# Kernel optimization log

Hardware: AMD Instinct MI355X
Metric: run time of the kernel (lower is better)

The kernel has to match this reference:

```python
import jax, jax.numpy as jnp
import numpy as np

B, N, D, D_OUT = 8, 2048, 1024, 1024

def setup_inputs() -> dict:
    key = jax.random.key(0)
    k1, k2, k3, k4, k5 = jax.random.split(key, 5)
    x = jax.random.normal(k1, (B, N, D), dtype=jnp.float32)
    # nn.Linear params: weight [out, in], bias [out]
    W_attn = jax.random.normal(k2, (D, D), dtype=jnp.float32) / np.sqrt(D)
    b_attn = jax.random.normal(k3, (D,), dtype=jnp.float32) * 0.01
    W_out = jax.random.normal(k4, (D_OUT, D), dtype=jnp.float32) / np.sqrt(D)
    b_out = jax.random.normal(k5, (D_OUT,), dtype=jnp.float32) * 0.01
    return {"x": x, "W_attn": W_attn, "b_attn": b_attn, "W_out": W_out, "b_out": b_out}

def reference(x, W_attn, b_attn, W_out, b_out):
    # query = x; key = attention_linear(x); value = output_linear(x)
    key = jnp.einsum('bnd,kd->bnk', x, W_attn) + b_attn   # [B,N,D]
    value = jnp.einsum('bnd,od->bno', x, W_out) + b_out   # [B,N,D_OUT]
    scale = 1.0 / np.sqrt(x.shape[-1]).astype(np.float32)
    scores = jnp.einsum('bqd,bkd->bqk', x, key) * scale   # [B,N,N]
    attn = jax.nn.softmax(scores, axis=-1)
    return jnp.einsum('bqk,bko->bqo', attn, value)        # [B,N,D_OUT]
```

## Files before the change

kernel.cpp:

```cpp
#include <hip/hip_runtime.h>
#include <hip/hip_bf16.h>
#include <cstdio>

typedef __bf16 bf16_t;
typedef __bf16 bf16x8 __attribute__((ext_vector_type(8)));
typedef __bf16 bf16x4 __attribute__((ext_vector_type(4)));
typedef float  f32x16 __attribute__((ext_vector_type(16)));

#define TM 128
#define TN 128
#define BK 32

__global__ __launch_bounds__(256)
void cvt_f32_bf16(const float* __restrict__ in, bf16_t* __restrict__ out, int n)
{
    for (int i = (blockIdx.x * 256 + threadIdx.x) * 4; i < n; i += gridDim.x * 256 * 4) {
        const float4 v = *(const float4*)(in + i);
        bf16x4 o;
        o[0] = (bf16_t)v.x; o[1] = (bf16_t)v.y; o[2] = (bf16_t)v.z; o[3] = (bf16_t)v.w;
        *(bf16x4*)(out + i) = o;
    }
}


__device__ __forceinline__ void stage_tiles(
    const bf16_t* __restrict__ Ab, const bf16_t* __restrict__ Bb,
    bf16_t* As, bf16_t* Bs, int k0, int K, int t, int w)
{
    const int src_c = (t & 3) ^ ((t >> 3) & 3);
#pragma unroll
    for (int rd = 0; rd < 2; rd++) {
        const int row = rd * 64 + (t >> 2);
        const bf16_t* ga = Ab + (size_t)row * K + k0 + src_c * 8;
        __builtin_amdgcn_global_load_lds(
            (const __attribute__((address_space(1))) void*)ga,
            (__attribute__((address_space(3))) void*)(&As[(rd * 64 + w * 16) * 32]),
            16, 0, 0);
        const bf16_t* gb = Bb + (size_t)row * K + k0 + src_c * 8;
        __builtin_amdgcn_global_load_lds(
            (const __attribute__((address_space(1))) void*)gb,
            (__attribute__((address_space(3))) void*)(&Bs[(rd * 64 + w * 16) * 32]),
            16, 0, 0);
    }
}

__device__ __forceinline__ int frag_idx(int row, int c)
{
    return row * 32 + ((c ^ ((row >> 1) & 3)) * 8);
}

template <int MODE>
__global__ __launch_bounds__(256)
void gemm_nt(const bf16_t* __restrict__ A, const bf16_t* __restrict__ Bm,
             void* __restrict__ Cv, float scale, int Ncols, int K,
             long long strideA, long long strideB, long long strideC,
             int tiles_m, int tiles_n)
{
    __shared__ bf16_t As[TM * BK];
    __shared__ bf16_t Bs[TN * BK];

    const int t    = threadIdx.x;
    const int w    = t >> 6;
    const int lane = t & 63;
    const int wm = w >> 1, wn = w & 1;
    const int lm = lane & 31;
    const int lk = lane >> 5;

    const int per_batch = tiles_m * tiles_n;
    const int batch = blockIdx.x / per_batch;
    const int rest  = blockIdx.x % per_batch;
    const int tm    = rest % tiles_m;
    const int tn    = rest / tiles_m;

    const bf16_t* Ab = A + (size_t)batch * strideA + (size_t)tm * TM * K;
    const bf16_t* Bb = Bm + (size_t)batch * strideB + (size_t)tn * TN * K;

    f32x16 acc[2][2];
#pragma unroll
    for (int i = 0; i < 2; i++)
#pragma unroll
        for (int j = 0; j < 2; j++)
#pragma unroll
            for (int e = 0; e < 16; e++) acc[i][j][e] = 0.f;

    for (int k0 = 0; k0 < K; k0 += BK) {
        stage_tiles(Ab, Bb, As, Bs, k0, K, t, w);
        __syncthreads();

        bf16x8 af[2][2], bf[2][2];
#pragma unroll
        for (int ks = 0; ks < 2; ks++) {
#pragma unroll
            for (int mt = 0; mt < 2; mt++)
                af[ks][mt] = *(const bf16x8*)&As[frag_idx(wm * 64 + mt * 32 + lm, ks * 2 + lk)];
#pragma unroll
            for (int nt = 0; nt < 2; nt++)
                bf[ks][nt] = *(const bf16x8*)&Bs[frag_idx(wn * 64 + nt * 32 + lm, ks * 2 + lk)];
        }
#pragma unroll
        for (int ks = 0; ks < 2; ks++)
#pragma unroll
            for (int mt = 0; mt < 2; mt++)
#pragma unroll
                for (int nt = 0; nt < 2; nt++)
                    acc[mt][nt] = __builtin_amdgcn_mfma_f32_32x32x16_bf16(
                        af[ks][mt], bf[ks][nt], acc[mt][nt], 0, 0, 0);
        __syncthreads();
    }

#pragma unroll
    for (int mt = 0; mt < 2; mt++)
#pragma unroll
        for (int nt = 0; nt < 2; nt++) {
            const int colg = tn * TN + wn * 64 + nt * 32 + lm;
#pragma unroll
            for (int rg = 0; rg < 4; rg++) {
                const int rowg = tm * TM + wm * 64 + mt * 32 + rg * 8 + 4 * lk;
                if (MODE == 2) {
                    bf16_t* p = (bf16_t*)Cv + (size_t)batch * strideC
                                  + (size_t)rowg * Ncols + colg;
#pragma unroll
                    for (int j = 0; j < 4; j++)
                        p[(size_t)j * Ncols] = (bf16_t)(acc[mt][nt][rg * 4 + j] * scale);
                } else {
                    float* p = (float*)Cv + (size_t)batch * strideC
                                  + (size_t)rowg * Ncols + colg;
#pragma unroll
                    for (int j = 0; j < 4; j++)
                        p[(size_t)j * Ncols] = acc[mt][nt][rg * 4 + j];
                }
            }
        }
}

__global__ __launch_bounds__(256)
void gemm_kv(const bf16_t* __restrict__ A,
             const bf16_t* __restrict__ Wa, const bf16_t* __restrict__ Wo,
             const float* __restrict__ ba, const float* __restrict__ bo,
             bf16_t* __restrict__ key, bf16_t* __restrict__ vT,
             int Nn, int Dd, int K)
{
    __shared__ bf16_t As[TM * BK];
    __shared__ bf16_t Bs[TN * BK];

    const int t    = threadIdx.x;
    const int w    = t >> 6;
    const int lane = t & 63;
    const int wm = w >> 1, wn = w & 1;
    const int lm = lane & 31;
    const int lk = lane >> 5;

    const int tiles_m = Nn / TM;
    const int per_batch = tiles_m * 16;
    const int batch = blockIdx.x / per_batch;
    const int rest  = blockIdx.x % per_batch;
    const int tm    = rest % tiles_m;
    const int tn    = rest / tiles_m;
    const bool isK  = (tn < 8);

    const bf16_t* Ab = A + (size_t)batch * Nn * K + (size_t)tm * TM * K;
    const bf16_t* Bb = (isK ? Wa + (size_t)tn * TN * K
                            : Wo + (size_t)(tn - 8) * TN * K);
    const float* bias = isK ? ba : bo;

    f32x16 acc[2][2];
#pragma unroll
    for (int i = 0; i < 2; i++)
#pragma unroll
        for (int j = 0; j < 2; j++)
#pragma unroll
            for (int e = 0; e < 16; e++) acc[i][j][e] = 0.f;

    for (int k0 = 0; k0 < K; k0 += BK) {
        stage_tiles(Ab, Bb, As, Bs, k0, K, t, w);
        __syncthreads();

        bf16x8 af[2][2], bf[2][2];
#pragma unroll
        for (int ks = 0; ks < 2; ks++) {
#pragma unroll
            for (int mt = 0; mt < 2; mt++)
                af[ks][mt] = *(const bf16x8*)&As[frag_idx(wm * 64 + mt * 32 + lm, ks * 2 + lk)];
#pragma unroll
            for (int nt = 0; nt < 2; nt++)
                bf[ks][nt] = *(const bf16x8*)&Bs[frag_idx(wn * 64 + nt * 32 + lm, ks * 2 + lk)];
        }
#pragma unroll
        for (int ks = 0; ks < 2; ks++)
#pragma unroll
            for (int mt = 0; mt < 2; mt++)
#pragma unroll
                for (int nt = 0; nt < 2; nt++)
                    acc[mt][nt] = __builtin_amdgcn_mfma_f32_32x32x16_bf16(
                        af[ks][mt], bf[ks][nt], acc[mt][nt], 0, 0, 0);
        __syncthreads();
    }

#pragma unroll
    for (int mt = 0; mt < 2; mt++)
#pragma unroll
        for (int nt = 0; nt < 2; nt++) {
            const int cw = (tn & 7) * TN + wn * 64 + nt * 32 + lm;
            const float bv = bias[cw];
#pragma unroll
            for (int rg = 0; rg < 4; rg++) {
                const int rowg = tm * TM + wm * 64 + mt * 32 + rg * 8 + 4 * lk;
                if (isK) {
                    bf16_t* p = key + (size_t)batch * Nn * Dd + (size_t)rowg * Dd + cw;
#pragma unroll
                    for (int j = 0; j < 4; j++)
                        p[(size_t)j * Dd] = (bf16_t)(acc[mt][nt][rg * 4 + j] + bv);
                } else {
                    bf16_t* p = vT + (size_t)batch * Dd * Nn + (size_t)cw * Nn + rowg;
                    bf16x4 pk;
#pragma unroll
                    for (int j = 0; j < 4; j++)
                        pk[j] = (bf16_t)(acc[mt][nt][rg * 4 + j] + bv);
                    *(bf16x4*)p = pk;
                }
            }
        }
}

__global__ __launch_bounds__(256)
void softmax_rows(bf16_t* __restrict__ S)
{
    __shared__ float red[8];
    const int t = threadIdx.x;
    const int w = t >> 6;
    const int lane = t & 63;
    bf16_t* p = S + (size_t)blockIdx.x * 2048;

    bf16x8 v = *(const bf16x8*)&p[t * 8];
    float x[8];
    float m = -1e30f;
#pragma unroll
    for (int i = 0; i < 8; i++) { x[i] = (float)v[i]; m = fmaxf(m, x[i]); }
#pragma unroll
    for (int off = 32; off >= 1; off >>= 1) m = fmaxf(m, __shfl_xor(m, off));
    if (lane == 0) red[w] = m;
    __syncthreads();
    m = fmaxf(fmaxf(red[0], red[1]), fmaxf(red[2], red[3]));

    float s = 0.f;
#pragma unroll
    for (int i = 0; i < 8; i++) { x[i] = __expf(x[i] - m); s += x[i]; }
#pragma unroll
    for (int off = 32; off >= 1; off >>= 1) s += __shfl_xor(s, off);
    if (lane == 0) red[4 + w] = s;
    __syncthreads();
    const float inv = 1.f / (red[4] + red[5] + red[6] + red[7]);

    bf16x8 o;
#pragma unroll
    for (int i = 0; i < 8; i++) o[i] = (bf16_t)(x[i] * inv);
    *(bf16x8*)&p[t * 8] = o;
}

extern "C" void kernel_launch(void* const* d_in, const int* in_sizes, int n_in,
                              void* d_out, int out_size, void* d_ws, size_t ws_size,
                              hipStream_t stream)
{
    const int Bn = 8, Nn = 2048, Dd = 1024;

    const float* x  = (const float*)d_in[0];
    const float* Wa = (const float*)d_in[1];
    const float* ba = (const float*)d_in[2];
    const float* Wo = (const float*)d_in[3];
    const float* bo = (const float*)d_in[4];
    float* out = (float*)d_out;

    const size_t nX = (size_t)Bn * Nn * Dd;
    const size_t nW = (size_t)Dd * Dd;
    const size_t nS = (size_t)Bn * Nn * Nn;

    bf16_t* xb  = (bf16_t*)d_ws;
    bf16_t* Wab = xb + nX;
    bf16_t* Wob = Wab + nW;
    bf16_t* key = Wob + nW;
    bf16_t* vT  = key + nX;
    bf16_t* S   = vT + nX;
    const size_t needed = (nX * 3 + nW * 2 + nS) * sizeof(bf16_t);
    if (ws_size < needed)
        fprintf(stderr, "kernel_launch: ws too small: have %zu need %zu\n", ws_size, needed);

    const dim3 blk(256);
    const long long sXN = (long long)Nn * Dd;
    const long long sS  = (long long)Nn * Nn;
    const long long sVT = (long long)Dd * Nn;

    cvt_f32_bf16<<<dim3(16384), blk, 0, stream>>>(x, xb, (int)nX);
    cvt_f32_bf16<<<dim3(1024), blk, 0, stream>>>(Wa, Wab, (int)nW);
    cvt_f32_bf16<<<dim3(1024), blk, 0, stream>>>(Wo, Wob, (int)nW);

    gemm_kv<<<dim3(Bn * 16 * 16), blk, 0, stream>>>(
        xb, Wab, Wob, ba, bo, key, vT, Nn, Dd, Dd);

    gemm_nt<2><<<dim3(Bn * 16 * 16), blk, 0, stream>>>(
        xb, key, S, 0.03125f, Nn, Dd, sXN, sXN, sS, 16, 16);

    softmax_rows<<<dim3(Bn * Nn), blk, 0, stream>>>(S);

    gemm_nt<3><<<dim3(Bn * 16 * 8), blk, 0, stream>>>(
        S, vT, (void*)out, 1.0f, Dd, Nn, sS, sVT, sXN, 16, 8);
}
```

Before: 427.4 us.

## Fuse softmax exp/normalize into PV GEMM and widen K-tile to 64

The softmax pass now only computes the row max and the reciprocal of the row sum, and no longer writes normalized probabilities back to S. The final GEMM recomputes exp(s - max) on the fly from the raw bf16 scores in shared memory and scales each output row by the reciprocal sum. This saves a full read-modify-write of the B×N×N score matrix. Separately, BK grows from 32 to 64 with a new 8-way XOR swizzle, which halves the number of K-loop iterations and barriers. In exchange, each PV tile re-evaluates exp on its A fragments once per column tile (8 times per row), and the doubled shared memory per block may lower occupancy.

After: 445.2 us. +4.2%, slower.

```diff
diff --git a/kernel.cpp b/kernel.cpp
--- a/kernel.cpp
+++ b/kernel.cpp
@@ -9,7 +9,7 @@
 
 #define TM 128
 #define TN 128
-#define BK 32
+#define BK 64
 
 __global__ __launch_bounds__(256)
 void cvt_f32_bf16(const float* __restrict__ in, bf16_t* __restrict__ out, int n)
@@ -22,39 +22,42 @@
     }
 }
 
-
-__device__ __forceinline__ void stage_tiles(
-    const bf16_t* __restrict__ Ab, const bf16_t* __restrict__ Bb,
-    bf16_t* As, bf16_t* Bs, int k0, int K, int t, int w)
-{
-    const int src_c = (t & 3) ^ ((t >> 3) & 3);
-#pragma unroll
-    for (int rd = 0; rd < 2; rd++) {
-        const int row = rd * 64 + (t >> 2);
-        const bf16_t* ga = Ab + (size_t)row * K + k0 + src_c * 8;
+__device__ __forceinline__ void stage2(const bf16_t* __restrict__ Ab,
+                                       const bf16_t* __restrict__ Bb,
+                                       bf16_t* As, bf16_t* Bs,
+                                       int k0, int K, int t, int w)
+{
+#pragma unroll
+    for (int p = 0; p < 4; p++) {
+        const int idx = p * 256 + t;
+        const int row = idx >> 3;
+        const int c   = (idx & 7) ^ (row & 7);
+        bf16_t* dstA = As + (p * 256 + w * 64) * 8;
+        bf16_t* dstB = Bs + (p * 256 + w * 64) * 8;
         __builtin_amdgcn_global_load_lds(
-            (const __attribute__((address_space(1))) void*)ga,
-            (__attribute__((address_space(3))) void*)(&As[(rd * 64 + w * 16) * 32]),
-            16, 0, 0);
-        const bf16_t* gb = Bb + (size_t)row * K + k0 + src_c * 8;
+            (const __attribute__((address_space(1))) void*)(Ab + (size_t)row * K + k0 + c * 8),
+            (__attribute__((address_space(3))) void*)dstA, 16, 0, 0);
         __builtin_amdgcn_global_load_lds(
-            (const __attribute__((address_space(1))) void*)gb,
-            (__attribute__((address_space(3))) void*)(&Bs[(rd * 64 + w * 16) * 32]),
-            16, 0, 0);
-    }
-}
-
-__device__ __forceinline__ int frag_idx(int row, int c)
-{
-    return row * 32 + ((c ^ ((row >> 1) & 3)) * 8);
-}
-
-template <int MODE>
-__global__ __launch_bounds__(256)
-void gemm_nt(const bf16_t* __restrict__ A, const bf16_t* __restrict__ Bm,
-             void* __restrict__ Cv, float scale, int Ncols, int K,
-             long long strideA, long long strideB, long long strideC,
-             int tiles_m, int tiles_n)
+            (const __attribute__((address_space(1))) void*)(Bb + (size_t)row * K + k0 + c * 8),
+            (__attribute__((address_space(3))) void*)dstB, 16, 0, 0);
+    }
+}
+
+__device__ __forceinline__ int fidx(int row, int c)
+{
+    return row * 64 + ((c ^ (row & 7)) * 8);
+}
+
+#define ACC_INIT(acc)                                            \
+    _Pragma("unroll") for (int i = 0; i < 2; i++)                \
+    _Pragma("unroll") for (int j = 0; j < 2; j++)                \
+    _Pragma("unroll") for (int e = 0; e < 16; e++) acc[i][j][e] = 0.f;
+
+__global__ __launch_bounds__(256)
+void gemm_scores(const bf16_t* __restrict__ A, const bf16_t* __restrict__ Bm,
+                 bf16_t* __restrict__ C, float scale, int Ncols, int K,
+                 long long strideA, long long strideB, long long strideC,
+                 int tiles_m, int tiles_n)
 {
     __shared__ bf16_t As[TM * BK];
     __shared__ bf16_t Bs[TN * BK];
@@ -76,35 +79,28 @@
     const bf16_t* Bb = Bm + (size_t)batch * strideB + (size_t)tn * TN * K;
 
     f32x16 acc[2][2];
-#pragma unroll
-    for (int i = 0; i < 2; i++)
-#pragma unroll
-        for (int j = 0; j < 2; j++)
-#pragma unroll
-            for (int e = 0; e < 16; e++) acc[i][j][e] = 0.f;
+    ACC_INIT(acc)
 
     for (int k0 = 0; k0 < K; k0 += BK) {
-        stage_tiles(Ab, Bb, As, Bs, k0, K, t, w);
-        __syncthreads();
-
-        bf16x8 af[2][2], bf[2][2];
-#pragma unroll
-        for (int ks = 0; ks < 2; ks++) {
-#pragma unroll
-            for (int mt = 0; mt < 2; mt++)
-                af[ks][mt] = *(const bf16x8*)&As[frag_idx(wm * 64 + mt * 32 + lm, ks * 2 + lk)];
+        stage2(Ab, Bb, As, Bs, k0, K, t, w);
+        __syncthreads();
+#pragma unroll
+        for (int ks = 0; ks < 4; ks++) {
+            const int c = ks * 2 + lk;
+            bf16x8 af[2], bf[2];
+#pragma unroll
+            for (int mt = 0; mt < 2; mt++)
+                af[mt] = *(const bf16x8*)&As[fidx(wm * 64 + mt * 32 + lm, c)];
 #pragma unroll
             for (int nt = 0; nt < 2; nt++)
-                bf[ks][nt] = *(const bf16x8*)&Bs[frag_idx(wn * 64 + nt * 32 + lm, ks * 2 + lk)];
-        }
-#pragma unroll
-        for (int ks = 0; ks < 2; ks++)
+                bf[nt] = *(const bf16x8*)&Bs[fidx(wn * 64 + nt * 32 + lm, c)];
 #pragma unroll
             for (int mt = 0; mt < 2; mt++)
 #pragma unroll
                 for (int nt = 0; nt < 2; nt++)
                     acc[mt][nt] = __builtin_amdgcn_mfma_f32_32x32x16_bf16(
-                        af[ks][mt], bf[ks][nt], acc[mt][nt], 0, 0, 0);
+                        af[mt], bf[nt], acc[mt][nt], 0, 0, 0);
+        }
         __syncthreads();
     }
 
@@ -116,19 +112,10 @@
 #pragma unroll
             for (int rg = 0; rg < 4; rg++) {
                 const int rowg = tm * TM + wm * 64 + mt * 32 + rg * 8 + 4 * lk;
-                if (MODE == 2) {
-                    bf16_t* p = (bf16_t*)Cv + (size_t)batch * strideC
-                                  + (size_t)rowg * Ncols + colg;
-#pragma unroll
-                    for (int j = 0; j < 4; j++)
-                        p[(size_t)j * Ncols] = (bf16_t)(acc[mt][nt][rg * 4 + j] * scale);
-                } else {
-                    float* p = (float*)Cv + (size_t)batch * strideC
-                                  + (size_t)rowg * Ncols + colg;
-#pragma unroll
-                    for (int j = 0; j < 4; j++)
-                        p[(size_t)j * Ncols] = acc[mt][nt][rg * 4 + j];
-                }
+                bf16_t* p = C + (size_t)batch * strideC + (size_t)rowg * Ncols + colg;
+#pragma unroll
+                for (int j = 0; j < 4; j++)
+                    p[(size_t)j * Ncols] = (bf16_t)(acc[mt][nt][rg * 4 + j] * scale);
             }
         }
 }
@@ -164,35 +151,28 @@
     const float* bias = isK ? ba : bo;
 
     f32x16 acc[2][2];
-#pragma unroll
-    for (int i = 0; i < 2; i++)
-#pragma unroll
-        for (int j = 0; j < 2; j++)
-#pragma unroll
-            for (int e = 0; e < 16; e++) acc[i][j][e] = 0.f;
+    ACC_INIT(acc)
 
     for (int k0 = 0; k0 < K; k0 += BK) {
-        stage_tiles(Ab, Bb, As, Bs, k0, K, t, w);
-        __syncthreads();
-
-        bf16x8 af[2][2], bf[2][2];
-#pragma unroll
-        for (int ks = 0; ks < 2; ks++) {
-#pragma unroll
-            for (int mt = 0; mt < 2; mt++)
-                af[ks][mt] = *(const bf16x8*)&As[frag_idx(wm * 64 + mt * 32 + lm, ks * 2 + lk)];
+        stage2(Ab, Bb, As, Bs, k0, K, t, w);
+        __syncthreads();
+#pragma unroll
+        for (int ks = 0; ks < 4; ks++) {
+            const int c = ks * 2 + lk;
+            bf16x8 af[2], bf[2];
+#pragma unroll
+            for (int mt = 0; mt < 2; mt++)
+                af[mt] = *(const bf16x8*)&As[fidx(wm * 64 + mt * 32 + lm, c)];
 #pragma unroll
             for (int nt = 0; nt < 2; nt++)
-                bf[ks][nt] = *(const bf16x8*)&Bs[frag_idx(wn * 64 + nt * 32 + lm, ks * 2 + lk)];
-        }
-#pragma unroll
-        for (int ks = 0; ks < 2; ks++)
+                bf[nt] = *(const bf16x8*)&Bs[fidx(wn * 64 + nt * 32 + lm, c)];
 #pragma unroll
             for (int mt = 0; mt < 2; mt++)
 #pragma unroll
                 for (int nt = 0; nt < 2; nt++)
                     acc[mt][nt] = __builtin_amdgcn_mfma_f32_32x32x16_bf16(
-                        af[ks][mt], bf[ks][nt], acc[mt][nt], 0, 0, 0);
+                        af[mt], bf[nt], acc[mt][nt], 0, 0, 0);
+        }
         __syncthreads();
     }
 
@@ -223,13 +203,14 @@
 }
 
 __global__ __launch_bounds__(256)
-void softmax_rows(bf16_t* __restrict__ S)
+void row_stats(const bf16_t* __restrict__ S, float* __restrict__ M,
+               float* __restrict__ RL)
 {
     __shared__ float red[8];
     const int t = threadIdx.x;
     const int w = t >> 6;
     const int lane = t & 63;
-    bf16_t* p = S + (size_t)blockIdx.x * 2048;
+    const bf16_t* p = S + (size_t)blockIdx.x * 2048;
 
     bf16x8 v = *(const bf16x8*)&p[t * 8];
     float x[8];
@@ -244,17 +225,96 @@
 
     float s = 0.f;
 #pragma unroll
-    for (int i = 0; i < 8; i++) { x[i] = __expf(x[i] - m); s += x[i]; }
+    for (int i = 0; i < 8; i++) s += __expf(x[i] - m);
 #pragma unroll
     for (int off = 32; off >= 1; off >>= 1) s += __shfl_xor(s, off);
     if (lane == 0) red[4 + w] = s;
     __syncthreads();
-    const float inv = 1.f / (red[4] + red[5] + red[6] + red[7]);
-
-    bf16x8 o;
-#pragma unroll
-    for (int i = 0; i < 8; i++) o[i] = (bf16_t)(x[i] * inv);
-    *(bf16x8*)&p[t * 8] = o;
+    if (t == 0) {
+        M[blockIdx.x]  = m;
+        RL[blockIdx.x] = 1.f / (red[4] + red[5] + red[6] + red[7]);
+    }
+}
+
+__global__ __launch_bounds__(256)
+void gemm_out(const bf16_t* __restrict__ S, const bf16_t* __restrict__ vT,
+              const float* __restrict__ M, const float* __restrict__ RL,
+              float* __restrict__ out, int Nn, int Dd)
+{
+    __shared__ bf16_t As[TM * BK];
+    __shared__ bf16_t Bs[TN * BK];
+
+    const int t    = threadIdx.x;
+    const int w    = t >> 6;
+    const int lane = t & 63;
+    const int wm = w >> 1, wn = w & 1;
+    const int lm = lane & 31;
+    const int lk = lane >> 5;
+
+    const int tiles_m = Nn / TM;
+    const int tiles_n = Dd / TN;
+    const int per_batch = tiles_m * tiles_n;
+    const int batch = blockIdx.x / per_batch;
+    const int rest  = blockIdx.x % per_batch;
+    const int tm    = rest % tiles_m;
+    const int tn    = rest / tiles_m;
+
+    const int K = Nn;
+    const bf16_t* Ab = S + (size_t)batch * Nn * Nn + (size_t)tm * TM * K;
+    const bf16_t* Bb = vT + (size_t)batch * Dd * Nn + (size_t)tn * TN * K;
+
+    float mr[2];
+#pragma unroll
+    for (int mt = 0; mt < 2; mt++)
+        mr[mt] = M[(size_t)batch * Nn + tm * TM + wm * 64 + mt * 32 + lm];
+
+    f32x16 acc[2][2];
+    ACC_INIT(acc)
+
+    for (int k0 = 0; k0 < K; k0 += BK) {
+        stage2(Ab, Bb, As, Bs, k0, K, t, w);
+        __syncthreads();
+#pragma unroll
+        for (int ks = 0; ks < 4; ks++) {
+            const int c = ks * 2 + lk;
+            bf16x8 af[2], bf[2];
+#pragma unroll
+            for (int mt = 0; mt < 2; mt++) {
+                bf16x8 raw = *(const bf16x8*)&As[fidx(wm * 64 + mt * 32 + lm, c)];
+                bf16x8 e;
+#pragma unroll
+                for (int j = 0; j < 8; j++)
+                    e[j] = (bf16_t)__expf((float)raw[j] - mr[mt]);
+                af[mt] = e;
+            }
+#pragma unroll
+            for (int nt = 0; nt < 2; nt++)
+                bf[nt] = *(const bf16x8*)&Bs[fidx(wn * 64 + nt * 32 + lm, c)];
+#pragma unroll
+            for (int mt = 0; mt < 2; mt++)
+#pragma unroll
+                for (int nt = 0; nt < 2; nt++)
+                    acc[mt][nt] = __builtin_amdgcn_mfma_f32_32x32x16_bf16(
+                        af[mt], bf[nt], acc[mt][nt], 0, 0, 0);
+        }
+        __syncthreads();
+    }
+
+#pragma unroll
+    for (int mt = 0; mt < 2; mt++)
+#pragma unroll
+        for (int nt = 0; nt < 2; nt++) {
+            const int colg = tn * TN + wn * 64 + nt * 32 + lm;
+#pragma unroll
+            for (int rg = 0; rg < 4; rg++) {
+                const int rowg = tm * TM + wm * 64 + mt * 32 + rg * 8 + 4 * lk;
+                const float* rlp = RL + (size_t)batch * Nn + rowg;
+                float* p = out + (size_t)batch * Nn * Dd + (size_t)rowg * Dd + colg;
+#pragma unroll
+                for (int j = 0; j < 4; j++)
+                    p[(size_t)j * Dd] = acc[mt][nt][rg * 4 + j] * rlp[j];
+            }
+        }
 }
 
 extern "C" void kernel_launch(void* const* d_in, const int* in_sizes, int n_in,
@@ -273,6 +333,7 @@
     const size_t nX = (size_t)Bn * Nn * Dd;
     const size_t nW = (size_t)Dd * Dd;
     const size_t nS = (size_t)Bn * Nn * Nn;
+    const size_t nR = (size_t)Bn * Nn;
 
     bf16_t* xb  = (bf16_t*)d_ws;
     bf16_t* Wab = xb + nX;
@@ -280,14 +341,15 @@
     bf16_t* key = Wob + nW;
     bf16_t* vT  = key + nX;
     bf16_t* S   = vT + nX;
-    const size_t needed = (nX * 3 + nW * 2 + nS) * sizeof(bf16_t);
+    float*  Mx  = (float*)(S + nS);
+    float*  RL  = Mx + nR;
+    const size_t needed = (nX * 3 + nW * 2 + nS) * sizeof(bf16_t) + 2 * nR * sizeof(float);
     if (ws_size < needed)
         fprintf(stderr, "kernel_launch: ws too small: have %zu need %zu\n", ws_size, needed);
 
     const dim3 blk(256);
     const long long sXN = (long long)Nn * Dd;
     const long long sS  = (long long)Nn * Nn;
-    const long long sVT = (long long)Dd * Nn;
 
     cvt_f32_bf16<<<dim3(16384), blk, 0, stream>>>(x, xb, (int)nX);
     cvt_f32_bf16<<<dim3(1024), blk, 0, stream>>>(Wa, Wab, (int)nW);
@@ -296,11 +358,11 @@
     gemm_kv<<<dim3(Bn * 16 * 16), blk, 0, stream>>>(
         xb, Wab, Wob, ba, bo, key, vT, Nn, Dd, Dd);
 
-    gemm_nt<2><<<dim3(Bn * 16 * 16), blk, 0, stream>>>(
+    gemm_scores<<<dim3(Bn * 16 * 16), blk, 0, stream>>>(
         xb, key, S, 0.03125f, Nn, Dd, sXN, sXN, sS, 16, 16);
 
-    softmax_rows<<<dim3(Bn * Nn), blk, 0, stream>>>(S);
-
-    gemm_nt<3><<<dim3(Bn * 16 * 8), blk, 0, stream>>>(
-        S, vT, (void*)out, 1.0f, Dd, Nn, sS, sVT, sXN, 16, 8);
-}
+    row_stats<<<dim3(Bn * Nn), blk, 0, stream>>>(S, Mx, RL);
+
+    gemm_out<<<dim3(Bn * 16 * 8), blk, 0, stream>>>(
+        S, vT, Mx, RL, out, Nn, Dd);
+}
```
